# Optimization experiments

Measured on AMD Instinct MI355X. Metric: run time of the kernel, lower is better.

The kernel has to match this reference:

```python
import jax, jax.numpy as jnp
import numpy as np
import math

B, S, D, H, W = 1, 2048, 512, 8, 64
DK = D // H
NEG = -1e9


def setup_inputs() -> dict:
    rng = jax.random.key(0)
    ks = jax.random.split(rng, 8)
    sc = 0.02
    return {
        "query": jax.random.normal(ks[0], (B, S, D), jnp.float32),
        "key": jax.random.normal(ks[1], (B, S, D), jnp.float32),
        "value": jax.random.normal(ks[2], (B, S, D), jnp.float32),
        "Wq": jax.random.normal(ks[3], (D, D), jnp.float32) * sc,
        "Wk": jax.random.normal(ks[4], (D, D), jnp.float32) * sc,
        "Wv": jax.random.normal(ks[5], (D, D), jnp.float32) * sc,
        "Wo": jax.random.normal(ks[6], (D, D), jnp.float32) * sc,
        "bo": jax.random.normal(ks[7], (D,), jnp.float32) * sc,
    }


def reference(query, key, value, Wq, Wk, Wv, Wo, bo):
    b, s, d = query.shape

    def proj(x, Wm):
        # [B,S,D] -> [B,H,S,DK]
        return (x @ Wm.T).reshape(b, s, H, DK).transpose(0, 2, 1, 3)

    Q = proj(query, Wq)
    K = proj(key, Wk)
    V = proj(value, Wv)

    i = jnp.arange(s)
    rel = jnp.arange(-W, 1)                     # causal band: keys i-W..i
    idx = i[:, None] + rel[None, :]             # [S, W+1]
    valid = idx >= 0
    idxc = jnp.clip(idx, 0, s - 1)

    Kw = K[:, :, idxc, :]                       # [B,H,S,W+1,DK]
    Vw = V[:, :, idxc, :]

    scores = jnp.einsum('bhsd,bhsrd->bhsr', Q, Kw) / math.sqrt(DK)
    decay_bias = 0.1 * jnp.exp(-0.1 * jnp.abs(rel.astype(jnp.float32)))
    scores = jnp.where(valid[None, None], scores + decay_bias, NEG)
    probs = jax.nn.softmax(scores, axis=-1)     # [B,H,S,W+1]

    out = jnp.einsum('bhsr,bhsrd->bhsd', probs, Vw)
    out = out.transpose(0, 2, 1, 3).reshape(b, s, d)
    output = out @ Wo.T + bo

    # attention_weights [B,H,S,2W]: only rows with window_size <= 2W are written
    win = jnp.minimum(s, i + W + 1) - jnp.maximum(0, i - W)   # [S]
    stored = win <= 2 * W
    slot = jnp.arange(2 * W)
    ridx = slot[None, :] + jnp.maximum(W - i, 0)[:, None]     # [S,2W] slot->band index
    vmask = (ridx <= W) & (slot[None, :] < win[:, None]) & stored[:, None]
    gath = jnp.take_along_axis(probs, jnp.clip(ridx, 0, W)[None, None], axis=-1)
    attn_w = jnp.where(vmask[None, None], gath, 0.0)

    return output, attn_w
```

## Files before the change

### kernel.cpp

```cpp
#include <hip/hip_runtime.h>
#include <stdint.h>

#define SEQ   2048
#define DM    512
#define NHEAD 8
#define DKH   64
#define WIN   64
#define NEGV  -1000000000.0f

typedef __attribute__((ext_vector_type(8))) short   short8;
typedef __attribute__((ext_vector_type(4))) float   float4v;
typedef __attribute__((ext_vector_type(8))) unsigned short ushort8v;

__device__ __forceinline__ unsigned short f2bf(float x) {
    uint32_t u = __float_as_uint(x);
    uint32_t r = (u + 0x7FFFu + ((u >> 16) & 1u)) >> 16;
    return (unsigned short)r;
}

__device__ __forceinline__ void async_cp16(const void* g, void* lds) {
    __builtin_amdgcn_global_load_lds(
        (const __attribute__((address_space(1))) unsigned int*)(uintptr_t)g,
        (__attribute__((address_space(3))) unsigned int*)(uint32_t)(uintptr_t)lds,
        16, 0, 0);
}

__global__ __launch_bounds__(256)
void cast7_kernel(const float* __restrict__ q, const float* __restrict__ k,
                  const float* __restrict__ v, const float* __restrict__ wq,
                  const float* __restrict__ wk, const float* __restrict__ wv,
                  const float* __restrict__ wo, unsigned short* __restrict__ dst)
{
    int g = (blockIdx.x * 256 + threadIdx.x) * 8;
    const float* src; int off;
    if      (g < 1048576) { src = q;  off = g; }
    else if (g < 2097152) { src = k;  off = g - 1048576; }
    else if (g < 3145728) { src = v;  off = g - 2097152; }
    else if (g < 3407872) { src = wq; off = g - 3145728; }
    else if (g < 3670016) { src = wk; off = g - 3407872; }
    else if (g < 3932160) { src = wv; off = g - 3670016; }
    else                  { src = wo; off = g - 3932160; }
    float4 x0 = *(const float4*)(src + off);
    float4 x1 = *(const float4*)(src + off + 4);
    ushort8v o;
    o[0] = f2bf(x0.x); o[1] = f2bf(x0.y); o[2] = f2bf(x0.z); o[3] = f2bf(x0.w);
    o[4] = f2bf(x1.x); o[5] = f2bf(x1.y); o[6] = f2bf(x1.z); o[7] = f2bf(x1.w);
    *(ushort8v*)(dst + g) = o;
}

template<bool BIAS>
__device__ __forceinline__ void gemm_mfma_body(const unsigned short* __restrict__ A,
                                               const unsigned short* __restrict__ B,
                                               const float* __restrict__ bias,
                                               float* __restrict__ C)
{
    __shared__ __align__(16) unsigned short As[128 * 32];
    __shared__ __align__(16) unsigned short Bs[128 * 32];

    const int tid  = threadIdx.x;
    const int m0   = blockIdx.x * 128;
    const int n0   = blockIdx.y * 128;
    const int lane = tid & 63;
    const int wave = tid >> 6;
    const int wm   = (wave >> 1) * 64;
    const int wn   = (wave & 1) * 64;
    const int lm   = lane & 15;
    const int lk   = (lane >> 4) * 8;

    float4v acc[4][4] = {};

    for (int k0 = 0; k0 < 512; k0 += 32) {
        #pragma unroll
        for (int h = 0; h < 2; h++) {
            int c  = tid + h * 256;
            int r  = c >> 2;
            int kc = (c & 3) * 8;
            async_cp16(A + (size_t)(m0 + r) * 512 + k0 + kc, As + c * 8);
            async_cp16(B + (size_t)(n0 + r) * 512 + k0 + kc, Bs + c * 8);
        }
        __syncthreads();

        short8 av[4], bv[4];
        #pragma unroll
        for (int mt = 0; mt < 4; mt++)
            av[mt] = *(const short8*)(As + (wm + mt * 16 + lm) * 32 + lk);
        #pragma unroll
        for (int nt = 0; nt < 4; nt++)
            bv[nt] = *(const short8*)(Bs + (wn + nt * 16 + lm) * 32 + lk);
        #pragma unroll
        for (int mt = 0; mt < 4; mt++)
            #pragma unroll
            for (int nt = 0; nt < 4; nt++)
                acc[mt][nt] = __builtin_amdgcn_mfma_f32_16x16x32_bf16(
                    av[mt], bv[nt], acc[mt][nt], 0, 0, 0);
        __syncthreads();
    }

    const int r0 = (lane >> 4) * 4;
    const int cn = lane & 15;
    #pragma unroll
    for (int nt = 0; nt < 4; nt++) {
        int gcol = n0 + wn + nt * 16 + cn;
        float b = BIAS ? bias[gcol] : 0.f;
        #pragma unroll
        for (int mt = 0; mt < 4; mt++) {
            int grow = m0 + wm + mt * 16 + r0;
            #pragma unroll
            for (int reg = 0; reg < 4; reg++)
                C[(size_t)(grow + reg) * 512 + gcol] = acc[mt][nt][reg] + b;
        }
    }
}

__global__ __launch_bounds__(256)
void qkv_gemm_kernel(const unsigned short* __restrict__ qb,
                     const unsigned short* __restrict__ kb,
                     const unsigned short* __restrict__ vb,
                     const unsigned short* __restrict__ wqb,
                     const unsigned short* __restrict__ wkb,
                     const unsigned short* __restrict__ wvb,
                     float* __restrict__ Qf, float* __restrict__ Kf,
                     float* __restrict__ Vf)
{
    const unsigned short *A, *B; float* C;
    if (blockIdx.z == 0)      { A = qb; B = wqb; C = Qf; }
    else if (blockIdx.z == 1) { A = kb; B = wkb; C = Kf; }
    else                      { A = vb; B = wvb; C = Vf; }
    gemm_mfma_body<false>(A, B, nullptr, C);
}

__global__ __launch_bounds__(256)
void out_gemm_kernel(const unsigned short* __restrict__ ctxb,
                     const unsigned short* __restrict__ wob,
                     const float* __restrict__ bo, float* __restrict__ out)
{
    gemm_mfma_body<true>(ctxb, wob, bo, out);
}

__global__ __launch_bounds__(256)
void attn_kernel(const float* __restrict__ Q, const float* __restrict__ K,
                 const float* __restrict__ V, unsigned short* __restrict__ ctxb,
                 float* __restrict__ attnw)
{
    __shared__ float Qs[16][68];
    __shared__ float Ks[80][68];
    __shared__ float Vs[80][68];
    __shared__ float Ps[16][66];

    const int h   = blockIdx.y;
    const int q0  = blockIdx.x * 16;
    const int tid = threadIdx.x;

    {
        int row = tid >> 4, c4 = (tid & 15) * 4;
        *(float4*)&Qs[row][c4] =
            *(const float4*)&Q[(q0 + row) * DM + h * DKH + c4];
    }
    for (int li = tid; li < 80 * 16; li += 256) {
        int row = li >> 4, c4 = (li & 15) * 4;
        int g = q0 - 64 + row;
        float4 kv = make_float4(0.f, 0.f, 0.f, 0.f);
        float4 vv = make_float4(0.f, 0.f, 0.f, 0.f);
        if (g >= 0) {
            kv = *(const float4*)&K[g * DM + h * DKH + c4];
            vv = *(const float4*)&V[g * DM + h * DKH + c4];
        }
        *(float4*)&Ks[row][c4] = kv;
        *(float4*)&Vs[row][c4] = vv;
    }
    __syncthreads();

    for (int t = tid; t < 16 * 65; t += 256) {
        int q = t / 65, r = t % 65;
        int g = q0 + q - 64 + r;
        float s = 0.f;
        #pragma unroll
        for (int x = 0; x < 64; x += 4) {
            float4 qa = *(const float4*)&Qs[q][x];
            float4 ka = *(const float4*)&Ks[q + r][x];
            s += qa.x * ka.x + qa.y * ka.y + qa.z * ka.z + qa.w * ka.w;
        }
        Ps[q][r] = (g >= 0)
            ? s * 0.125f + 0.1f * __expf(-0.1f * (float)(64 - r))
            : NEGV;
    }
    __syncthreads();

    {
        int wave = tid >> 6;
        int lane = tid & 63;
        for (int q = wave; q < 16; q += 4) {
            float v    = Ps[q][lane];
            float v64  = Ps[q][64];
            float m = v;
            #pragma unroll
            for (int off = 32; off >= 1; off >>= 1)
                m = fmaxf(m, __shfl_xor(m, off));
            m = fmaxf(m, v64);
            float e   = __expf(v - m);
            float e64 = __expf(v64 - m);
            float ssum = e;
            #pragma unroll
            for (int off = 32; off >= 1; off >>= 1)
                ssum += __shfl_xor(ssum, off);
            ssum += e64;
            float inv = 1.f / ssum;
            Ps[q][lane] = e * inv;
            if (lane == 0) Ps[q][64] = e64 * inv;
        }
    }
    __syncthreads();

    {
        int q  = tid >> 4;
        int c4 = (tid & 15) * 4;
        float4 o = make_float4(0.f, 0.f, 0.f, 0.f);
        for (int r = 0; r <= 64; r++) {
            float p = Ps[q][r];
            float4 vv = *(const float4*)&Vs[q + r][c4];
            o.x += p * vv.x; o.y += p * vv.y;
            o.z += p * vv.z; o.w += p * vv.w;
        }
        ushort4 o4 = make_ushort4(f2bf(o.x), f2bf(o.y), f2bf(o.z), f2bf(o.w));
        *(ushort4*)&ctxb[(q0 + q) * DM + h * DKH + c4] = o4;
    }

    for (int t = tid; t < 16 * 128; t += 256) {
        int q = t >> 7, slot = t & 127;
        int i = q0 + q;
        float val = 0.f;
        if (i < WIN) {
            if (slot <= i) val = Ps[q][slot + WIN - i];
        } else if (i >= SEQ - WIN) {
            if (slot <= WIN) val = Ps[q][slot];
        }
        attnw[(h * SEQ + i) * 2 * WIN + slot] = val;
    }
}

extern "C" void kernel_launch(void* const* d_in, const int* in_sizes, int n_in,
                              void* d_out, int out_size, void* d_ws, size_t ws_size,
                              hipStream_t stream)
{
    const float* query = (const float*)d_in[0];
    const float* key   = (const float*)d_in[1];
    const float* value = (const float*)d_in[2];
    const float* Wq    = (const float*)d_in[3];
    const float* Wk    = (const float*)d_in[4];
    const float* Wv    = (const float*)d_in[5];
    const float* Wo    = (const float*)d_in[6];
    const float* bo    = (const float*)d_in[7];

    float* out   = (float*)d_out;
    float* attnw = out + SEQ * DM;

    unsigned short* qb   = (unsigned short*)d_ws;
    unsigned short* kb   = qb  + 1048576;
    unsigned short* vb   = kb  + 1048576;
    unsigned short* wqb  = vb  + 1048576;
    unsigned short* wkb  = wqb + 262144;
    unsigned short* wvb  = wkb + 262144;
    unsigned short* wob  = wvb + 262144;
    unsigned short* ctxb = wob + 262144;
    float* Qf = (float*)(ctxb + 1048576);
    float* Kf = Qf + 1048576;
    float* Vf = Kf + 1048576;

    cast7_kernel<<<2048, 256, 0, stream>>>(query, key, value, Wq, Wk, Wv, Wo, qb);

    dim3 g1(SEQ / 128, DM / 128, 3);
    qkv_gemm_kernel<<<g1, 256, 0, stream>>>(qb, kb, vb, wqb, wkb, wvb, Qf, Kf, Vf);

    dim3 g2(SEQ / 16, NHEAD);
    attn_kernel<<<g2, 256, 0, stream>>>(Qf, Kf, Vf, ctxb, attnw);

    dim3 g3(SEQ / 128, DM / 128);
    out_gemm_kernel<<<g3, 256, 0, stream>>>(ctxb, wob, bo, out);
}
```

Measured before the change: 127.4 us.

## Store Q/K/V in bf16 and compute banded attention with MFMA tiles

```diff
diff --git a/kernel.cpp b/kernel.cpp
--- a/kernel.cpp
+++ b/kernel.cpp
@@ -8,14 +8,17 @@
 #define WIN   64
 #define NEGV  -1000000000.0f
 
-typedef __attribute__((ext_vector_type(8))) short   short8;
-typedef __attribute__((ext_vector_type(4))) float   float4v;
+typedef __attribute__((ext_vector_type(8))) short          short8;
+typedef __attribute__((ext_vector_type(4))) float          float4v;
 typedef __attribute__((ext_vector_type(8))) unsigned short ushort8v;
 
 __device__ __forceinline__ unsigned short f2bf(float x) {
     uint32_t u = __float_as_uint(x);
     uint32_t r = (u + 0x7FFFu + ((u >> 16) & 1u)) >> 16;
     return (unsigned short)r;
+}
+__device__ __forceinline__ float bf2f(unsigned short u) {
+    return __uint_as_float(((uint32_t)u) << 16);
 }
 
 __device__ __forceinline__ void async_cp16(const void* g, void* lds) {
@@ -48,11 +51,11 @@
     *(ushort8v*)(dst + g) = o;
 }
 
-template<bool BIAS>
+template<bool BIAS, bool OUT_BF16>
 __device__ __forceinline__ void gemm_mfma_body(const unsigned short* __restrict__ A,
                                                const unsigned short* __restrict__ B,
                                                const float* __restrict__ bias,
-                                               float* __restrict__ C)
+                                               void* __restrict__ Cv)
 {
     __shared__ __align__(16) unsigned short As[128 * 32];
     __shared__ __align__(16) unsigned short Bs[128 * 32];
@@ -106,8 +109,13 @@
         for (int mt = 0; mt < 4; mt++) {
             int grow = m0 + wm + mt * 16 + r0;
             #pragma unroll
-            for (int reg = 0; reg < 4; reg++)
-                C[(size_t)(grow + reg) * 512 + gcol] = acc[mt][nt][reg] + b;
+            for (int reg = 0; reg < 4; reg++) {
+                float val = acc[mt][nt][reg] + b;
+                if (OUT_BF16)
+                    ((unsigned short*)Cv)[(size_t)(grow + reg) * 512 + gcol] = f2bf(val);
+                else
+                    ((float*)Cv)[(size_t)(grow + reg) * 512 + gcol] = val;
+            }
         }
     }
 }
@@ -119,14 +127,14 @@
                      const unsigned short* __restrict__ wqb,
                      const unsigned short* __restrict__ wkb,
                      const unsigned short* __restrict__ wvb,
-                     float* __restrict__ Qf, float* __restrict__ Kf,
-                     float* __restrict__ Vf)
-{
-    const unsigned short *A, *B; float* C;
-    if (blockIdx.z == 0)      { A = qb; B = wqb; C = Qf; }
-    else if (blockIdx.z == 1) { A = kb; B = wkb; C = Kf; }
-    else                      { A = vb; B = wvb; C = Vf; }
-    gemm_mfma_body<false>(A, B, nullptr, C);
+                     unsigned short* __restrict__ Qp, unsigned short* __restrict__ Kp,
+                     unsigned short* __restrict__ Vp)
+{
+    const unsigned short *A, *B; unsigned short* C;
+    if (blockIdx.z == 0)      { A = qb; B = wqb; C = Qp; }
+    else if (blockIdx.z == 1) { A = kb; B = wkb; C = Kp; }
+    else                      { A = vb; B = wvb; C = Vp; }
+    gemm_mfma_body<false, true>(A, B, nullptr, C);
 }
 
 __global__ __launch_bounds__(256)
@@ -134,107 +142,175 @@
                      const unsigned short* __restrict__ wob,
                      const float* __restrict__ bo, float* __restrict__ out)
 {
-    gemm_mfma_body<true>(ctxb, wob, bo, out);
+    gemm_mfma_body<true, false>(ctxb, wob, bo, out);
 }
 
 __global__ __launch_bounds__(256)
-void attn_kernel(const float* __restrict__ Q, const float* __restrict__ K,
-                 const float* __restrict__ V, unsigned short* __restrict__ ctxb,
+void attn_kernel(const unsigned short* __restrict__ Qp,
+                 const unsigned short* __restrict__ Kp,
+                 const unsigned short* __restrict__ Vp,
+                 unsigned short* __restrict__ ctxb,
                  float* __restrict__ attnw)
 {
-    __shared__ float Qs[16][68];
-    __shared__ float Ks[80][68];
-    __shared__ float Vs[80][68];
-    __shared__ float Ps[16][66];
+    __shared__ __align__(16) unsigned short Qs[64 * 72];
+    __shared__ __align__(16) unsigned short Ks[128 * 72];
+    __shared__ __align__(16) unsigned short Vt[64 * 136];
+    __shared__ __align__(16) unsigned short Ps[4][16][96];
 
     const int h   = blockIdx.y;
-    const int q0  = blockIdx.x * 16;
+    const int q0  = blockIdx.x * 64;
     const int tid = threadIdx.x;
 
+    for (int c = tid; c < 512; c += 256) {
+        int row = c >> 3, ch = c & 7;
+        *(ushort8v*)&Qs[row * 72 + ch * 8] =
+            *(const ushort8v*)&Qp[(size_t)(q0 + row) * 512 + h * 64 + ch * 8];
+    }
+    for (int c = tid; c < 1024; c += 256) {
+        int row = c >> 3, ch = c & 7;
+        int g = q0 - 64 + row;
+        ushort8v val = {0, 0, 0, 0, 0, 0, 0, 0};
+        if (g >= 0)
+            val = *(const ushort8v*)&Kp[(size_t)g * 512 + h * 64 + ch * 8];
+        *(ushort8v*)&Ks[row * 72 + ch * 8] = val;
+    }
     {
-        int row = tid >> 4, c4 = (tid & 15) * 4;
-        *(float4*)&Qs[row][c4] =
-            *(const float4*)&Q[(q0 + row) * DM + h * DKH + c4];
-    }
-    for (int li = tid; li < 80 * 16; li += 256) {
-        int row = li >> 4, c4 = (li & 15) * 4;
-        int g = q0 - 64 + row;
-        float4 kv = make_float4(0.f, 0.f, 0.f, 0.f);
-        float4 vv = make_float4(0.f, 0.f, 0.f, 0.f);
-        if (g >= 0) {
-            kv = *(const float4*)&K[g * DM + h * DKH + c4];
-            vv = *(const float4*)&V[g * DM + h * DKH + c4];
-        }
-        *(float4*)&Ks[row][c4] = kv;
-        *(float4*)&Vs[row][c4] = vv;
+        int key = tid >> 1, dh = tid & 1;
+        int g = q0 - 64 + key;
+        ushort8v vv[4];
+        #pragma unroll
+        for (int j = 0; j < 4; j++) {
+            ushort8v z = {0, 0, 0, 0, 0, 0, 0, 0};
+            vv[j] = (g >= 0)
+                ? *(const ushort8v*)&Vp[(size_t)g * 512 + h * 64 + dh * 32 + j * 8]
+                : z;
+        }
+        #pragma unroll
+        for (int j = 0; j < 4; j++)
+            #pragma unroll
+            for (int e = 0; e < 8; e++)
+                Vt[(dh * 32 + j * 8 + e) * 136 + key] = vv[j][e];
     }
     __syncthreads();
 
-    for (int t = tid; t < 16 * 65; t += 256) {
-        int q = t / 65, r = t % 65;
-        int g = q0 + q - 64 + r;
+    const int lane = tid & 63;
+    const int w    = tid >> 6;
+    const int lm   = lane & 15;
+    const int g16  = lane >> 4;
+    const int lk8  = g16 * 8;
+
+    short8 av0 = *(const short8*)&Qs[(w * 16 + lm) * 72 + lk8];
+    short8 av1 = *(const short8*)&Qs[(w * 16 + lm) * 72 + 32 + lk8];
+    float4v sc[5];
+    #pragma unroll
+    for (int kt = 0; kt < 5; kt++) {
+        const unsigned short* kr = &Ks[(w * 16 + kt * 16 + lm) * 72];
+        short8 b0 = *(const short8*)(kr + lk8);
+        short8 b1 = *(const short8*)(kr + 32 + lk8);
+        float4v a = {0.f, 0.f, 0.f, 0.f};
+        a = __builtin_amdgcn_mfma_f32_16x16x32_bf16(av0, b0, a, 0, 0, 0);
+        a = __builtin_amdgcn_mfma_f32_16x16x32_bf16(av1, b1, a, 0, 0, 0);
+        sc[kt] = a;
+    }
+
+    float v[5][4];
+    #pragma unroll
+    for (int kt = 0; kt < 5; kt++) {
+        int kk = kt * 16 + lm;
+        int g  = q0 - 64 + w * 16 + kk;
+        #pragma unroll
+        for (int reg = 0; reg < 4; reg++) {
+            int r = g16 * 4 + reg;
+            bool valid = (kk >= r) && (kk <= r + 64) && (g >= 0);
+            v[kt][reg] = valid
+                ? sc[kt][reg] * 0.125f + 0.1f * __expf(-0.1f * (float)(64 + r - kk))
+                : NEGV;
+        }
+    }
+
+    float mx[4], sm[4];
+    #pragma unroll
+    for (int reg = 0; reg < 4; reg++) {
+        float m = v[0][reg];
+        #pragma unroll
+        for (int kt = 1; kt < 5; kt++) m = fmaxf(m, v[kt][reg]);
+        mx[reg] = m;
+    }
+    #pragma unroll
+    for (int off = 1; off < 16; off <<= 1)
+        #pragma unroll
+        for (int reg = 0; reg < 4; reg++)
+            mx[reg] = fmaxf(mx[reg], __shfl_xor(mx[reg], off));
+    float p[5][4];
+    #pragma unroll
+    for (int reg = 0; reg < 4; reg++) {
         float s = 0.f;
         #pragma unroll
-        for (int x = 0; x < 64; x += 4) {
-            float4 qa = *(const float4*)&Qs[q][x];
-            float4 ka = *(const float4*)&Ks[q + r][x];
-            s += qa.x * ka.x + qa.y * ka.y + qa.z * ka.z + qa.w * ka.w;
-        }
-        Ps[q][r] = (g >= 0)
-            ? s * 0.125f + 0.1f * __expf(-0.1f * (float)(64 - r))
-            : NEGV;
-    }
+        for (int kt = 0; kt < 5; kt++) {
+            float e = __expf(v[kt][reg] - mx[reg]);
+            p[kt][reg] = e;
+            s += e;
+        }
+        sm[reg] = s;
+    }
+    #pragma unroll
+    for (int off = 1; off < 16; off <<= 1)
+        #pragma unroll
+        for (int reg = 0; reg < 4; reg++)
+            sm[reg] += __shfl_xor(sm[reg], off);
+    #pragma unroll
+    for (int reg = 0; reg < 4; reg++) {
+        float inv = 1.f / sm[reg];
+        #pragma unroll
+        for (int kt = 0; kt < 5; kt++) p[kt][reg] *= inv;
+    }
+
+    #pragma unroll
+    for (int kt = 0; kt < 5; kt++)
+        #pragma unroll
+        for (int reg = 0; reg < 4; reg++)
+            Ps[w][g16 * 4 + reg][kt * 16 + lm] = f2bf(p[kt][reg]);
+    #pragma unroll
+    for (int reg = 0; reg < 4; reg++)
+        Ps[w][g16 * 4 + reg][80 + lm] = 0;
+
+    float4v oacc[4] = {};
+    #pragma unroll
+    for (int ks = 0; ks < 3; ks++) {
+        short8 pa = *(const short8*)&Ps[w][lm][ks * 32 + lk8];
+        #pragma unroll
+        for (int nt = 0; nt < 4; nt++) {
+            short8 vb = *(const short8*)&Vt[(nt * 16 + lm) * 136 + w * 16 + ks * 32 + lk8];
+            oacc[nt] = __builtin_amdgcn_mfma_f32_16x16x32_bf16(pa, vb, oacc[nt], 0, 0, 0);
+        }
+    }
+
+    #pragma unroll
+    for (int nt = 0; nt < 4; nt++)
+        #pragma unroll
+        for (int reg = 0; reg < 4; reg++) {
+            int i = q0 + w * 16 + g16 * 4 + reg;
+            ctxb[(size_t)i * 512 + h * 64 + nt * 16 + lm] = f2bf(oacc[nt][reg]);
+        }
+
     __syncthreads();
 
-    {
-        int wave = tid >> 6;
-        int lane = tid & 63;
-        for (int q = wave; q < 16; q += 4) {
-            float v    = Ps[q][lane];
-            float v64  = Ps[q][64];
-            float m = v;
-            #pragma unroll
-            for (int off = 32; off >= 1; off >>= 1)
-                m = fmaxf(m, __shfl_xor(m, off));
-            m = fmaxf(m, v64);
-            float e   = __expf(v - m);
-            float e64 = __expf(v64 - m);
-            float ssum = e;
-            #pragma unroll
-            for (int off = 32; off >= 1; off >>= 1)
-                ssum += __shfl_xor(ssum, off);
-            ssum += e64;
-            float inv = 1.f / ssum;
-            Ps[q][lane] = e * inv;
-            if (lane == 0) Ps[q][64] = e64 * inv;
-        }
-    }
-    __syncthreads();
-
-    {
-        int q  = tid >> 4;
-        int c4 = (tid & 15) * 4;
-        float4 o = make_float4(0.f, 0.f, 0.f, 0.f);
-        for (int r = 0; r <= 64; r++) {
-            float p = Ps[q][r];
-            float4 vv = *(const float4*)&Vs[q + r][c4];
-            o.x += p * vv.x; o.y += p * vv.y;
-            o.z += p * vv.z; o.w += p * vv.w;
-        }
-        ushort4 o4 = make_ushort4(f2bf(o.x), f2bf(o.y), f2bf(o.z), f2bf(o.w));
-        *(ushort4*)&ctxb[(q0 + q) * DM + h * DKH + c4] = o4;
-    }
-
-    for (int t = tid; t < 16 * 128; t += 256) {
-        int q = t >> 7, slot = t & 127;
-        int i = q0 + q;
+    for (int t = tid; t < 64 * 128; t += 256) {
+        int ql = t >> 7, slot = t & 127;
+        int i  = q0 + ql;
         float val = 0.f;
-        if (i < WIN) {
-            if (slot <= i) val = Ps[q][slot + WIN - i];
-        } else if (i >= SEQ - WIN) {
-            if (slot <= WIN) val = Ps[q][slot];
-        }
-        attnw[(h * SEQ + i) * 2 * WIN + slot] = val;
+        if (q0 == 0) {
+            if (slot <= ql) {
+                int kk = (ql & 15) + slot + 64 - ql;
+                val = bf2f(Ps[ql >> 4][ql & 15][kk]);
+            }
+        } else if (q0 == SEQ - 64) {
+            if (slot <= 64) {
+                int kk = (ql & 15) + slot;
+                val = bf2f(Ps[ql >> 4][ql & 15][kk]);
+            }
+        }
+        attnw[((size_t)h * SEQ + i) * 2 * WIN + slot] = val;
     }
 }
 
@@ -261,18 +337,18 @@
     unsigned short* wkb  = wqb + 262144;
     unsigned short* wvb  = wkb + 262144;
     unsigned short* wob  = wvb + 262144;
-    unsigned short* ctxb = wob + 262144;
-    float* Qf = (float*)(ctxb + 1048576);
-    float* Kf = Qf + 1048576;
-    float* Vf = Kf + 1048576;
+    unsigned short* Qp   = wob + 262144;
+    unsigned short* Kp   = Qp  + 1048576;
+    unsigned short* Vp   = Kp  + 1048576;
+    unsigned short* ctxb = Vp  + 1048576;
 
     cast7_kernel<<<2048, 256, 0, stream>>>(query, key, value, Wq, Wk, Wv, Wo, qb);
 
     dim3 g1(SEQ / 128, DM / 128, 3);
-    qkv_gemm_kernel<<<g1, 256, 0, stream>>>(qb, kb, vb, wqb, wkb, wvb, Qf, Kf, Vf);
-
-    dim3 g2(SEQ / 16, NHEAD);
-    attn_kernel<<<g2, 256, 0, stream>>>(Qf, Kf, Vf, ctxb, attnw);
+    qkv_gemm_kernel<<<g1, 256, 0, stream>>>(qb, kb, vb, wqb, wkb, wvb, Qp, Kp, Vp);
+
+    dim3 g2(SEQ / 64, NHEAD);
+    attn_kernel<<<g2, 256, 0, stream>>>(Qp, Kp, Vp, ctxb, attnw);
 
     dim3 g3(SEQ / 128, DM / 128);
     out_gemm_kernel<<<g3, 256, 0, stream>>>(ctxb, wob, bo, out);
```

Measured after the change: 113.8 us. 10.7% less time.
